# Kernel tuning notes

Measured on AMD Instinct MI355X. Metric: run time of the kernel, lower is better.

The kernel has to match this reference:

```python
import jax, jax.numpy as jnp
import numpy as np

N = 50000          # number of parent nodes / neighborhoods
D_IN = 256         # input_size
K = 8              # points decoded per neighborhood
GLOBAL_DIMS = [256, 128, 64]
FC_DIMS = [256, 256, 256]


def _linear_params(key, d_in, d_out):
    kw, kb = jax.random.split(key)
    W = jax.random.normal(kw, (d_in, d_out), dtype=jnp.float32) * 0.05
    b = jax.random.normal(kb, (d_out,), dtype=jnp.float32) * 0.05
    return W, b


def setup_inputs() -> dict:
    key = jax.random.key(0)
    keys = jax.random.split(key, 8)
    inp = {"input_features": jax.random.normal(keys[0], (N, D_IN), dtype=jnp.float32)}
    # global MLP: 256 -> 256 -> 128 -> 64
    d = D_IN
    for i, nb in enumerate(GLOBAL_DIMS):
        W, b = _linear_params(keys[1 + i], d, nb)
        inp[f"Wg{i}"], inp[f"bg{i}"] = W, b
        d = nb
    # neighborhood decoder head: 64 -> K*3
    inp["Wdec"], inp["bdec"] = _linear_params(keys[4], GLOBAL_DIMS[-1], K * 3)
    # per-point MLP: (256 + 64 + 3) -> 256 -> 256 -> 256
    d = D_IN + GLOBAL_DIMS[-1] + 3
    for i, nb in enumerate(FC_DIMS):
        W, b = _linear_params(keys[5 + i], d, nb)
        inp[f"W{i}"], inp[f"b{i}"] = W, b
        d = nb
    return inp


def reference(input_features, Wg0, bg0, Wg1, bg1, Wg2, bg2, Wdec, bdec,
              W0, b0, W1, b1, W2, b2):
    relu = jax.nn.relu
    # global feature MLP on node features: [N, 256] -> [N, 64]
    feats = input_features
    for W, b in ((Wg0, bg0), (Wg1, bg1), (Wg2, bg2)):
        feats = relu(feats @ W + b)
    # neighborhood decoder: K relative 3D points per node -> [N*K, 3]
    relative_points = (feats @ Wdec + bdec).reshape(-1, 3)
    cluster = jnp.repeat(jnp.arange(N, dtype=jnp.int32), K)  # [N*K]
    # gather (duplicate) parent features per decoded point
    nbr_dup = jnp.take(feats, cluster, axis=0)               # [N*K, 64]
    inp_dup = jnp.take(input_features, cluster, axis=0)      # [N*K, 256]
    decoded = jnp.concatenate([inp_dup, nbr_dup, relative_points], axis=1)  # [N*K, 323]
    for W, b in ((W0, b0), (W1, b1), (W2, b2)):
        decoded = relu(decoded @ W + b)
    return relative_points, decoded, cluster
```

## Files before the change

### kernel.cpp

```cpp
#include <hip/hip_runtime.h>
#include <hip/hip_bf16.h>

typedef __attribute__((ext_vector_type(8))) __bf16 bf16x8;
typedef __attribute__((ext_vector_type(4))) float f32x4;
typedef __attribute__((ext_vector_type(4))) unsigned short u16x4;

#define NN 50000
#define TM1 16
#define PNODES 16

#define FEATS_OFF 212992
#define GW_OFF    3412992

__device__ __forceinline__ unsigned short f2bf(float f) {
    unsigned int u = __builtin_bit_cast(unsigned int, f);
    u = (u + 0x7FFFu + ((u >> 16) & 1u)) >> 16;
    return (unsigned short)u;
}
__device__ __forceinline__ float bf2f(unsigned short h) {
    return __builtin_bit_cast(float, (unsigned int)h << 16);
}

__global__ __launch_bounds__(256) void k_prep(
    const float* __restrict__ W0, const float* __restrict__ W1,
    const float* __restrict__ W2,
    const float* __restrict__ Wg0, const float* __restrict__ Wg1,
    const float* __restrict__ Wg2,
    unsigned short* __restrict__ wbf)
{
    int idx = blockIdx.x * 256 + threadIdx.x;
    if (idx < 81920) {
        int n = idx / 320, k = idx - n * 320;
        wbf[idx] = f2bf(W0[(size_t)k * 256 + n]);
    } else if (idx < 147456) {
        int e = idx - 81920;
        int n = e >> 8, k = e & 255;
        wbf[idx] = f2bf(W1[(size_t)k * 256 + n]);
    } else if (idx < 212992) {
        int e = idx - 147456;
        int n = e >> 8, k = e & 255;
        wbf[idx] = f2bf(W2[(size_t)k * 256 + n]);
    } else if (idx < 319488) {
        int e = idx - 212992;
        float v; int oh, ol;
        if (e < 65536) {
            int n = e >> 8, k = e & 255;
            v = Wg0[(size_t)k * 256 + n];
            oh = GW_OFF + e; ol = GW_OFF + 65536 + e;
        } else if (e < 98304) {
            int e2 = e - 65536;
            int n = e2 >> 8, k = e2 & 255;
            v = Wg1[(size_t)k * 128 + n];
            oh = GW_OFF + 131072 + e2; ol = GW_OFF + 163840 + e2;
        } else {
            int e3 = e - 98304;
            int n = e3 >> 7, k = e3 & 127;
            v = Wg2[(size_t)k * 64 + n];
            oh = GW_OFF + 196608 + e3; ol = GW_OFF + 204800 + e3;
        }
        unsigned short h = f2bf(v);
        wbf[oh] = h;
        wbf[ol] = f2bf(v - bf2f(h));
    }
}

__global__ __launch_bounds__(256, 6) void k_global(
    const float* __restrict__ x,
    const float* __restrict__ bg0, const float* __restrict__ bg1,
    const float* __restrict__ bg2,
    const float* __restrict__ Wdec, const float* __restrict__ bdec,
    const unsigned short* __restrict__ gw,
    unsigned short* __restrict__ feats_bf,
    float* __restrict__ out_rel,
    float* __restrict__ out_cluster)
{
    __shared__ __attribute__((aligned(16))) unsigned char smem[25600];
    unsigned short* bufA = (unsigned short*)(smem);
    unsigned short* bufB = (unsigned short*)(smem + 8448);
    unsigned short* q1h  = (unsigned short*)(smem + 16896);
    unsigned short* q1l  = (unsigned short*)(smem + 21248);
    float*          g2   = (float*)(smem + 16896);

    const int tid  = threadIdx.x;
    const int lane = tid & 63;
    const int w    = tid >> 6;
    const int quad = lane >> 4;
    const int l15  = lane & 15;
    const int blk  = blockIdx.x;

    {
        const float4* xg = (const float4*)(x + (size_t)blk * TM1 * 256);
        #pragma unroll
        for (int it = 0; it < 4; ++it) {
            int e = tid + it * 256;
            int r = e >> 6, c4 = e & 63;
            float4 v = xg[e];
            u16x4 hv, lv;
            hv[0] = f2bf(v.x); lv[0] = f2bf(v.x - bf2f(hv[0]));
            hv[1] = f2bf(v.y); lv[1] = f2bf(v.y - bf2f(hv[1]));
            hv[2] = f2bf(v.z); lv[2] = f2bf(v.z - bf2f(hv[2]));
            hv[3] = f2bf(v.w); lv[3] = f2bf(v.w - bf2f(hv[3]));
            *(u16x4*)&bufA[r * 264 + c4 * 4] = hv;
            *(u16x4*)&bufB[r * 264 + c4 * 4] = lv;
        }
    }
    __syncthreads();

    f32x4 accL0[4];
    {
        const unsigned short* Wh = gw;
        const unsigned short* Wl = gw + 65536;
        f32x4 z = {0.f, 0.f, 0.f, 0.f};
        #pragma unroll
        for (int t = 0; t < 4; ++t) accL0[t] = z;
        #pragma unroll
        for (int ks = 0; ks < 8; ++ks) {
            int k0 = ks * 32 + quad * 8;
            bf16x8 ah = *(const bf16x8*)&bufA[l15 * 264 + k0];
            bf16x8 al = *(const bf16x8*)&bufB[l15 * 264 + k0];
            bf16x8 bh[4], bl[4];
            #pragma unroll
            for (int t = 0; t < 4; ++t) {
                int n = w * 64 + t * 16 + l15;
                bh[t] = *(const bf16x8*)(Wh + (size_t)n * 256 + k0);
                bl[t] = *(const bf16x8*)(Wl + (size_t)n * 256 + k0);
            }
            #pragma unroll
            for (int t = 0; t < 4; ++t) {
                accL0[t] = __builtin_amdgcn_mfma_f32_16x16x32_bf16(ah, bh[t], accL0[t], 0, 0, 0);
                accL0[t] = __builtin_amdgcn_mfma_f32_16x16x32_bf16(al, bh[t], accL0[t], 0, 0, 0);
                accL0[t] = __builtin_amdgcn_mfma_f32_16x16x32_bf16(ah, bl[t], accL0[t], 0, 0, 0);
            }
        }
    }
    __syncthreads();

    {
        #pragma unroll
        for (int t = 0; t < 4; ++t) {
            int col = w * 64 + t * 16 + l15;
            float bb = bg0[col];
            #pragma unroll
            for (int r = 0; r < 4; ++r) {
                int row = quad * 4 + r;
                float v = fmaxf(accL0[t][r] + bb, 0.f);
                unsigned short h = f2bf(v);
                bufA[row * 264 + col] = h;
                bufB[row * 264 + col] = f2bf(v - bf2f(h));
            }
        }
    }
    __syncthreads();

    {
        const unsigned short* Wh = gw + 131072;
        const unsigned short* Wl = gw + 163840;
        f32x4 acc[2];
        f32x4 z = {0.f, 0.f, 0.f, 0.f};
        acc[0] = z; acc[1] = z;
        #pragma unroll
        for (int ks = 0; ks < 8; ++ks) {
            int k0 = ks * 32 + quad * 8;
            bf16x8 ah = *(const bf16x8*)&bufA[l15 * 264 + k0];
            bf16x8 al = *(const bf16x8*)&bufB[l15 * 264 + k0];
            bf16x8 bh[2], bl[2];
            #pragma unroll
            for (int t = 0; t < 2; ++t) {
                int n = w * 32 + t * 16 + l15;
                bh[t] = *(const bf16x8*)(Wh + (size_t)n * 256 + k0);
                bl[t] = *(const bf16x8*)(Wl + (size_t)n * 256 + k0);
            }
            #pragma unroll
            for (int t = 0; t < 2; ++t) {
                acc[t] = __builtin_amdgcn_mfma_f32_16x16x32_bf16(ah, bh[t], acc[t], 0, 0, 0);
                acc[t] = __builtin_amdgcn_mfma_f32_16x16x32_bf16(al, bh[t], acc[t], 0, 0, 0);
                acc[t] = __builtin_amdgcn_mfma_f32_16x16x32_bf16(ah, bl[t], acc[t], 0, 0, 0);
            }
        }
        #pragma unroll
        for (int t = 0; t < 2; ++t) {
            int col = w * 32 + t * 16 + l15;
            float bb = bg1[col];
            #pragma unroll
            for (int r = 0; r < 4; ++r) {
                int row = quad * 4 + r;
                float v = fmaxf(acc[t][r] + bb, 0.f);
                unsigned short h = f2bf(v);
                q1h[row * 136 + col] = h;
                q1l[row * 136 + col] = f2bf(v - bf2f(h));
            }
        }
    }
    __syncthreads();

    f32x4 accL2;
    {
        const unsigned short* Wh = gw + 196608;
        const unsigned short* Wl = gw + 204800;
        f32x4 z = {0.f, 0.f, 0.f, 0.f};
        accL2 = z;
        #pragma unroll
        for (int ks = 0; ks < 4; ++ks) {
            int k0 = ks * 32 + quad * 8;
            bf16x8 ah = *(const bf16x8*)&q1h[l15 * 136 + k0];
            bf16x8 al = *(const bf16x8*)&q1l[l15 * 136 + k0];
            int n = w * 16 + l15;
            bf16x8 bh = *(const bf16x8*)(Wh + (size_t)n * 128 + k0);
            bf16x8 bl = *(const bf16x8*)(Wl + (size_t)n * 128 + k0);
            accL2 = __builtin_amdgcn_mfma_f32_16x16x32_bf16(ah, bh, accL2, 0, 0, 0);
            accL2 = __builtin_amdgcn_mfma_f32_16x16x32_bf16(al, bh, accL2, 0, 0, 0);
            accL2 = __builtin_amdgcn_mfma_f32_16x16x32_bf16(ah, bl, accL2, 0, 0, 0);
        }
    }
    __syncthreads();

    {
        int col = w * 16 + l15;
        float bb = bg2[col];
        #pragma unroll
        for (int r = 0; r < 4; ++r) {
            int row = quad * 4 + r;
            g2[row * 64 + col] = fmaxf(accL2[r] + bb, 0.f);
        }
    }
    __syncthreads();

    {
        const float* src = g2 + tid * 4;
        u16x4 p;
        p[0] = f2bf(src[0]); p[1] = f2bf(src[1]);
        p[2] = f2bf(src[2]); p[3] = f2bf(src[3]);
        *(u16x4*)&feats_bf[(size_t)blk * (TM1 * 64) + tid * 4] = p;
    }

    for (int tt = tid; tt < TM1 * 24; tt += 256) {
        int m = tt / 24;
        int c = tt - m * 24;
        float acc = bdec[c];
        for (int i = 0; i < 64; ++i) acc += g2[m * 64 + i] * Wdec[i * 24 + c];
        out_rel[(size_t)blk * (TM1 * 24) + tt] = acc;
    }

    if (tid < TM1 * 8) {
        out_cluster[(size_t)blk * (TM1 * 8) + tid] = (float)(blk * TM1 + (tid >> 3));
    }
}

__global__ __launch_bounds__(512, 4) void k_points(
    const float* __restrict__ x,
    const unsigned short* __restrict__ feats_bf,
    const float* __restrict__ rel_in,
    const unsigned short* __restrict__ wbf,
    const float* __restrict__ W0f,
    const float* __restrict__ b0,
    const float* __restrict__ b1,
    const float* __restrict__ b2,
    float* __restrict__ out_dec)
{
    __shared__ __attribute__((aligned(16))) unsigned char smem[70144];
    unsigned char*  hB   = smem;
    unsigned short* xcat = (unsigned short*)smem;
    float*          sp   = (float*)(smem + 49152);
    float*          w3   = (float*)(smem + 65536);
    float*          rl   = (float*)(smem + 68608);

    const int tid  = threadIdx.x;
    const int lane = tid & 63;
    const int w    = tid >> 6;
    const int wr   = w >> 2;
    const int wc   = w & 3;
    const int quad = lane >> 4;
    const int l15  = lane & 15;
    const int blk  = blockIdx.x;
    const size_t nb = (size_t)blk * PNODES;

    {
        const float4* xg = (const float4*)(x + nb * 256);
        #pragma unroll
        for (int it = 0; it < 2; ++it) {
            int e = tid + it * 512;
            int r = e >> 6, c4 = e & 63;
            float4 v = xg[e];
            u16x4 hv;
            hv[0] = f2bf(v.x); hv[1] = f2bf(v.y);
            hv[2] = f2bf(v.z); hv[3] = f2bf(v.w);
            *(u16x4*)&xcat[r * 336 + c4 * 4] = hv;
        }
        {
            int e = tid * 2;
            int r = e >> 6, c = e & 63;
            *(unsigned int*)&xcat[r * 336 + 256 + c] =
                *(const unsigned int*)&feats_bf[nb * 64 + e];
        }
        for (int e = tid; e < 768; e += 512)
            w3[e] = W0f[(size_t)(320 + (e >> 8)) * 256 + (e & 255)];
        if (tid < 384) rl[tid] = rel_in[nb * 24 + tid];
    }
    __syncthreads();

    {
        const unsigned short* W0t = wbf;
        f32x4 acc[2];
        f32x4 z = {0.f, 0.f, 0.f, 0.f};
        acc[0] = z; acc[1] = z;
        bf16x8 bcur[2], bnxt[2];
        #pragma unroll
        for (int t = 0; t < 2; ++t)
            bcur[t] = *(const bf16x8*)(W0t + (size_t)(w * 32 + t * 16 + l15) * 320 + quad * 8);
        #pragma unroll
        for (int ks = 0; ks < 10; ++ks) {
            int k0 = ks * 32 + quad * 8;
            bf16x8 a = *(const bf16x8*)&xcat[l15 * 336 + k0];
            if (ks < 9) {
                #pragma unroll
                for (int t = 0; t < 2; ++t)
                    bnxt[t] = *(const bf16x8*)(W0t + (size_t)(w * 32 + t * 16 + l15) * 320 + k0 + 32);
            }
            #pragma unroll
            for (int t = 0; t < 2; ++t)
                acc[t] = __builtin_amdgcn_mfma_f32_16x16x32_bf16(a, bcur[t], acc[t], 0, 0, 0);
            if (ks < 9) {
                #pragma unroll
                for (int t = 0; t < 2; ++t) bcur[t] = bnxt[t];
            }
        }
        #pragma unroll
        for (int t = 0; t < 2; ++t) {
            int col = w * 32 + t * 16 + l15;
            float bb = b0[col];
            #pragma unroll
            for (int r = 0; r < 4; ++r) {
                int row = quad * 4 + r;
                sp[row * 256 + col] = acc[t][r] + bb;
            }
        }
    }
    __syncthreads();

    {
        float4 sv0 = *(const float4*)&sp[(2 * w) * 256 + lane * 4];
        float4 sv1 = *(const float4*)&sp[(2 * w + 1) * 256 + lane * 4];
        float4 wa  = *(const float4*)&w3[lane * 4];
        float4 wb4 = *(const float4*)&w3[256 + lane * 4];
        float4 wc4 = *(const float4*)&w3[512 + lane * 4];
        __syncthreads();
        #pragma unroll
        for (int it = 0; it < 16; ++it) {
            int row  = w * 16 + it;
            int node = 2 * w + (it >> 3);
            int p    = it & 7;
            float4 sv = (it < 8) ? sv0 : sv1;
            float ra = rl[node * 24 + p * 3 + 0];
            float rb = rl[node * 24 + p * 3 + 1];
            float rc = rl[node * 24 + p * 3 + 2];
            float v0 = fmaxf(sv.x + ra * wa.x + rb * wb4.x + rc * wc4.x, 0.f);
            float v1 = fmaxf(sv.y + ra * wa.y + rb * wb4.y + rc * wc4.y, 0.f);
            float v2 = fmaxf(sv.z + ra * wa.z + rb * wb4.z + rc * wc4.z, 0.f);
            float v3 = fmaxf(sv.w + ra * wa.w + rb * wb4.w + rc * wc4.w, 0.f);
            unsigned int lo = (unsigned int)f2bf(v0) | ((unsigned int)f2bf(v1) << 16);
            unsigned int hi = (unsigned int)f2bf(v2) | ((unsigned int)f2bf(v3) << 16);
            uint2 pk; pk.x = lo; pk.y = hi;
            int byteoff = row * 512 +
                ((((lane >> 1) ^ (row & 7)) << 4) | ((lane & 1) << 3));
            *(uint2*)(hB + byteoff) = pk;
        }
    }
    __syncthreads();

    {
        const unsigned short* W1t = wbf + 81920;
        f32x4 acc[4][4];
        f32x4 z = {0.f, 0.f, 0.f, 0.f};
        #pragma unroll
        for (int m = 0; m < 4; ++m)
            #pragma unroll
            for (int t = 0; t < 4; ++t) acc[m][t] = z;
        bf16x8 bcur[4], bnxt[4];
        #pragma unroll
        for (int t = 0; t < 4; ++t)
            bcur[t] = *(const bf16x8*)(W1t + (size_t)(wc * 64 + t * 16 + l15) * 256 + quad * 8);
        #pragma unroll
        for (int ks = 0; ks < 8; ++ks) {
            int k0 = ks * 32 + quad * 8;
            int g  = k0 >> 3;
            bf16x8 a[4];
            #pragma unroll
            for (int m = 0; m < 4; ++m) {
                int row = wr * 64 + m * 16 + l15;
                a[m] = *(const bf16x8*)(hB + row * 512 + ((g ^ (row & 7)) << 4));
            }
            if (ks < 7) {
                #pragma unroll
                for (int t = 0; t < 4; ++t)
                    bnxt[t] = *(const bf16x8*)(W1t + (size_t)(wc * 64 + t * 16 + l15) * 256 + k0 + 32);
            }
            #pragma unroll
            for (int m = 0; m < 4; ++m)
                #pragma unroll
                for (int t = 0; t < 4; ++t)
                    acc[m][t] = __builtin_amdgcn_mfma_f32_16x16x32_bf16(a[m], bcur[t], acc[m][t], 0, 0, 0);
            if (ks < 7) {
                #pragma unroll
                for (int t = 0; t < 4; ++t) bcur[t] = bnxt[t];
            }
        }
        __syncthreads();
        #pragma unroll
        for (int t = 0; t < 4; ++t) {
            int col = wc * 64 + t * 16 + l15;
            float bb = b1[col];
            #pragma unroll
            for (int m = 0; m < 4; ++m) {
                #pragma unroll
                for (int r = 0; r < 4; ++r) {
                    int row = wr * 64 + m * 16 + quad * 4 + r;
                    int byteoff = row * 512 +
                        ((((col >> 3) ^ (row & 7)) << 4) | ((col & 7) << 1));
                    *(unsigned short*)(hB + byteoff) =
                        f2bf(fmaxf(acc[m][t][r] + bb, 0.f));
                }
            }
        }
    }
    __syncthreads();

    {
        const unsigned short* W2t = wbf + 147456;
        f32x4 acc[4][4];
        f32x4 z = {0.f, 0.f, 0.f, 0.f};
        #pragma unroll
        for (int m = 0; m < 4; ++m)
            #pragma unroll
            for (int t = 0; t < 4; ++t) acc[m][t] = z;
        bf16x8 bcur[4], bnxt[4];
        #pragma unroll
        for (int t = 0; t < 4; ++t)
            bcur[t] = *(const bf16x8*)(W2t + (size_t)(wc * 64 + t * 16 + l15) * 256 + quad * 8);
        #pragma unroll
        for (int ks = 0; ks < 8; ++ks) {
            int k0 = ks * 32 + quad * 8;
            int g  = k0 >> 3;
            bf16x8 a[4];
            #pragma unroll
            for (int m = 0; m < 4; ++m) {
                int row = wr * 64 + m * 16 + l15;
                a[m] = *(const bf16x8*)(hB + row * 512 + ((g ^ (row & 7)) << 4));
            }
            if (ks < 7) {
                #pragma unroll
                for (int t = 0; t < 4; ++t)
                    bnxt[t] = *(const bf16x8*)(W2t + (size_t)(wc * 64 + t * 16 + l15) * 256 + k0 + 32);
            }
            #pragma unroll
            for (int m = 0; m < 4; ++m)
                #pragma unroll
                for (int t = 0; t < 4; ++t)
                    acc[m][t] = __builtin_amdgcn_mfma_f32_16x16x32_bf16(a[m], bcur[t], acc[m][t], 0, 0, 0);
            if (ks < 7) {
                #pragma unroll
                for (int t = 0; t < 4; ++t) bcur[t] = bnxt[t];
            }
        }
        #pragma unroll
        for (int t = 0; t < 4; ++t) {
            int col = wc * 64 + t * 16 + l15;
            float bb = b2[col];
            #pragma unroll
            for (int m = 0; m < 4; ++m) {
                #pragma unroll
                for (int r = 0; r < 4; ++r) {
                    int row = wr * 64 + m * 16 + quad * 4 + r;
                    out_dec[((size_t)blk * 128 + row) * 256 + col] =
                        fmaxf(acc[m][t][r] + bb, 0.f);
                }
            }
        }
    }
}

extern "C" void kernel_launch(void* const* d_in, const int* in_sizes, int n_in,
                              void* d_out, int out_size, void* d_ws, size_t ws_size,
                              hipStream_t stream) {
    const float* x    = (const float*)d_in[0];
    const float* Wg0  = (const float*)d_in[1];
    const float* bg0  = (const float*)d_in[2];
    const float* Wg1  = (const float*)d_in[3];
    const float* bg1  = (const float*)d_in[4];
    const float* Wg2  = (const float*)d_in[5];
    const float* bg2  = (const float*)d_in[6];
    const float* Wdec = (const float*)d_in[7];
    const float* bdec = (const float*)d_in[8];
    const float* W0   = (const float*)d_in[9];
    const float* b0   = (const float*)d_in[10];
    const float* W1   = (const float*)d_in[11];
    const float* b1   = (const float*)d_in[12];
    const float* W2   = (const float*)d_in[13];
    const float* b2   = (const float*)d_in[14];

    float* out      = (float*)d_out;
    float* out_rel  = out;
    float* out_dec  = out + 1200000;
    float* out_clu  = out + 103600000;

    unsigned short* wbf      = (unsigned short*)d_ws;
    unsigned short* feats_bf = wbf + FEATS_OFF;
    unsigned short* gw       = wbf + GW_OFF;

    k_prep<<<1248, 256, 0, stream>>>(W0, W1, W2, Wg0, Wg1, Wg2, wbf);
    k_global<<<NN / TM1, 256, 0, stream>>>(x, bg0, bg1, bg2, Wdec, bdec, gw,
                                           feats_bf, out_rel, out_clu);
    k_points<<<NN / PNODES, 512, 0, stream>>>(x, feats_bf, out_rel,
                                              wbf, W0, b0, b1, b2, out_dec);
}
```

Measured before the change: 876.5 us.

## Give each wave its own 16-node tile in global MLP, removing block barriers

The global MLP kernel now assigns a full 16-node tile to each wavefront, and each wave computes every output column with private LDS buffers. Before, the block's four waves split the columns of one shared tile. This removes all __syncthreads between layers and cuts the grid to 782 blocks. The trade-offs are far more accumulator registers per wave (16 tiles for layer 0), launch bounds lowered to allow that, larger shared memory per block, and every wave re-reading the full weight matrices from cache. The decoder dot product is also vectorized with float4 reads of g2.

```diff
diff --git a/kernel.cpp b/kernel.cpp
--- a/kernel.cpp
+++ b/kernel.cpp
@@ -6,7 +6,6 @@
 typedef __attribute__((ext_vector_type(4))) unsigned short u16x4;
 
 #define NN 50000
-#define TM1 16
 #define PNODES 16
 
 #define FEATS_OFF 212992
@@ -64,7 +63,7 @@
     }
 }
 
-__global__ __launch_bounds__(256, 6) void k_global(
+__global__ __launch_bounds__(256, 2) void k_global(
     const float* __restrict__ x,
     const float* __restrict__ bg0, const float* __restrict__ bg1,
     const float* __restrict__ bg2,
@@ -74,25 +73,26 @@
     float* __restrict__ out_rel,
     float* __restrict__ out_cluster)
 {
-    __shared__ __attribute__((aligned(16))) unsigned char smem[25600];
-    unsigned short* bufA = (unsigned short*)(smem);
-    unsigned short* bufB = (unsigned short*)(smem + 8448);
-    unsigned short* q1h  = (unsigned short*)(smem + 16896);
-    unsigned short* q1l  = (unsigned short*)(smem + 21248);
-    float*          g2   = (float*)(smem + 16896);
+    __shared__ __attribute__((aligned(16))) unsigned char smem[67584];
 
     const int tid  = threadIdx.x;
     const int lane = tid & 63;
     const int w    = tid >> 6;
     const int quad = lane >> 4;
     const int l15  = lane & 15;
-    const int blk  = blockIdx.x;
-
-    {
-        const float4* xg = (const float4*)(x + (size_t)blk * TM1 * 256);
-        #pragma unroll
-        for (int it = 0; it < 4; ++it) {
-            int e = tid + it * 256;
+    const int gwid = blockIdx.x * 4 + w;
+    if (gwid >= 3125) return;
+    const size_t node_base = (size_t)gwid * 16;
+
+    unsigned char* wbase = smem + (size_t)w * 16896;
+    unsigned short* A = (unsigned short*)wbase;
+    unsigned short* B = (unsigned short*)(wbase + 8448);
+
+    {
+        const float4* xg = (const float4*)(x + node_base * 256);
+        #pragma unroll
+        for (int it = 0; it < 16; ++it) {
+            int e = lane + it * 64;
             int r = e >> 6, c4 = e & 63;
             float4 v = xg[e];
             u16x4 hv, lv;
@@ -100,149 +100,147 @@
             hv[1] = f2bf(v.y); lv[1] = f2bf(v.y - bf2f(hv[1]));
             hv[2] = f2bf(v.z); lv[2] = f2bf(v.z - bf2f(hv[2]));
             hv[3] = f2bf(v.w); lv[3] = f2bf(v.w - bf2f(hv[3]));
-            *(u16x4*)&bufA[r * 264 + c4 * 4] = hv;
-            *(u16x4*)&bufB[r * 264 + c4 * 4] = lv;
-        }
-    }
-    __syncthreads();
-
-    f32x4 accL0[4];
+            *(u16x4*)&A[r * 264 + c4 * 4] = hv;
+            *(u16x4*)&B[r * 264 + c4 * 4] = lv;
+        }
+    }
+
     {
         const unsigned short* Wh = gw;
         const unsigned short* Wl = gw + 65536;
+        f32x4 acc[16];
         f32x4 z = {0.f, 0.f, 0.f, 0.f};
         #pragma unroll
-        for (int t = 0; t < 4; ++t) accL0[t] = z;
-        #pragma unroll
+        for (int t = 0; t < 16; ++t) acc[t] = z;
+        #pragma unroll 2
         for (int ks = 0; ks < 8; ++ks) {
             int k0 = ks * 32 + quad * 8;
-            bf16x8 ah = *(const bf16x8*)&bufA[l15 * 264 + k0];
-            bf16x8 al = *(const bf16x8*)&bufB[l15 * 264 + k0];
-            bf16x8 bh[4], bl[4];
-            #pragma unroll
-            for (int t = 0; t < 4; ++t) {
-                int n = w * 64 + t * 16 + l15;
-                bh[t] = *(const bf16x8*)(Wh + (size_t)n * 256 + k0);
-                bl[t] = *(const bf16x8*)(Wl + (size_t)n * 256 + k0);
-            }
-            #pragma unroll
-            for (int t = 0; t < 4; ++t) {
-                accL0[t] = __builtin_amdgcn_mfma_f32_16x16x32_bf16(ah, bh[t], accL0[t], 0, 0, 0);
-                accL0[t] = __builtin_amdgcn_mfma_f32_16x16x32_bf16(al, bh[t], accL0[t], 0, 0, 0);
-                accL0[t] = __builtin_amdgcn_mfma_f32_16x16x32_bf16(ah, bl[t], accL0[t], 0, 0, 0);
-            }
-        }
-    }
-    __syncthreads();
-
-    {
-        #pragma unroll
-        for (int t = 0; t < 4; ++t) {
-            int col = w * 64 + t * 16 + l15;
+            bf16x8 ah = *(const bf16x8*)&A[l15 * 264 + k0];
+            bf16x8 al = *(const bf16x8*)&B[l15 * 264 + k0];
+            #pragma unroll
+            for (int t = 0; t < 16; ++t) {
+                int n = t * 16 + l15;
+                bf16x8 bh = *(const bf16x8*)(Wh + (size_t)n * 256 + k0);
+                bf16x8 bl = *(const bf16x8*)(Wl + (size_t)n * 256 + k0);
+                acc[t] = __builtin_amdgcn_mfma_f32_16x16x32_bf16(ah, bh, acc[t], 0, 0, 0);
+                acc[t] = __builtin_amdgcn_mfma_f32_16x16x32_bf16(al, bh, acc[t], 0, 0, 0);
+                acc[t] = __builtin_amdgcn_mfma_f32_16x16x32_bf16(ah, bl, acc[t], 0, 0, 0);
+            }
+        }
+        #pragma unroll
+        for (int t = 0; t < 16; ++t) {
+            int col = t * 16 + l15;
             float bb = bg0[col];
-            #pragma unroll
-            for (int r = 0; r < 4; ++r) {
-                int row = quad * 4 + r;
-                float v = fmaxf(accL0[t][r] + bb, 0.f);
-                unsigned short h = f2bf(v);
-                bufA[row * 264 + col] = h;
-                bufB[row * 264 + col] = f2bf(v - bf2f(h));
-            }
-        }
-    }
-    __syncthreads();
-
-    {
-        const unsigned short* Wh = gw + 131072;
-        const unsigned short* Wl = gw + 163840;
-        f32x4 acc[2];
-        f32x4 z = {0.f, 0.f, 0.f, 0.f};
-        acc[0] = z; acc[1] = z;
-        #pragma unroll
-        for (int ks = 0; ks < 8; ++ks) {
-            int k0 = ks * 32 + quad * 8;
-            bf16x8 ah = *(const bf16x8*)&bufA[l15 * 264 + k0];
-            bf16x8 al = *(const bf16x8*)&bufB[l15 * 264 + k0];
-            bf16x8 bh[2], bl[2];
-            #pragma unroll
-            for (int t = 0; t < 2; ++t) {
-                int n = w * 32 + t * 16 + l15;
-                bh[t] = *(const bf16x8*)(Wh + (size_t)n * 256 + k0);
-                bl[t] = *(const bf16x8*)(Wl + (size_t)n * 256 + k0);
-            }
-            #pragma unroll
-            for (int t = 0; t < 2; ++t) {
-                acc[t] = __builtin_amdgcn_mfma_f32_16x16x32_bf16(ah, bh[t], acc[t], 0, 0, 0);
-                acc[t] = __builtin_amdgcn_mfma_f32_16x16x32_bf16(al, bh[t], acc[t], 0, 0, 0);
-                acc[t] = __builtin_amdgcn_mfma_f32_16x16x32_bf16(ah, bl[t], acc[t], 0, 0, 0);
-            }
-        }
-        #pragma unroll
-        for (int t = 0; t < 2; ++t) {
-            int col = w * 32 + t * 16 + l15;
-            float bb = bg1[col];
             #pragma unroll
             for (int r = 0; r < 4; ++r) {
                 int row = quad * 4 + r;
                 float v = fmaxf(acc[t][r] + bb, 0.f);
                 unsigned short h = f2bf(v);
-                q1h[row * 136 + col] = h;
-                q1l[row * 136 + col] = f2bf(v - bf2f(h));
-            }
-        }
-    }
-    __syncthreads();
-
-    f32x4 accL2;
+                A[row * 264 + col] = h;
+                B[row * 264 + col] = f2bf(v - bf2f(h));
+            }
+        }
+    }
+
+    {
+        const unsigned short* Wh = gw + 131072;
+        const unsigned short* Wl = gw + 163840;
+        f32x4 acc[8];
+        f32x4 z = {0.f, 0.f, 0.f, 0.f};
+        #pragma unroll
+        for (int t = 0; t < 8; ++t) acc[t] = z;
+        #pragma unroll 2
+        for (int ks = 0; ks < 8; ++ks) {
+            int k0 = ks * 32 + quad * 8;
+            bf16x8 ah = *(const bf16x8*)&A[l15 * 264 + k0];
+            bf16x8 al = *(const bf16x8*)&B[l15 * 264 + k0];
+            #pragma unroll
+            for (int t = 0; t < 8; ++t) {
+                int n = t * 16 + l15;
+                bf16x8 bh = *(const bf16x8*)(Wh + (size_t)n * 256 + k0);
+                bf16x8 bl = *(const bf16x8*)(Wl + (size_t)n * 256 + k0);
+                acc[t] = __builtin_amdgcn_mfma_f32_16x16x32_bf16(ah, bh, acc[t], 0, 0, 0);
+                acc[t] = __builtin_amdgcn_mfma_f32_16x16x32_bf16(al, bh, acc[t], 0, 0, 0);
+                acc[t] = __builtin_amdgcn_mfma_f32_16x16x32_bf16(ah, bl, acc[t], 0, 0, 0);
+            }
+        }
+        #pragma unroll
+        for (int t = 0; t < 8; ++t) {
+            int col = t * 16 + l15;
+            float bb = bg1[col];
+            #pragma unroll
+            for (int r = 0; r < 4; ++r) {
+                int row = quad * 4 + r;
+                float v = fmaxf(acc[t][r] + bb, 0.f);
+                unsigned short h = f2bf(v);
+                A[row * 136 + col] = h;
+                B[row * 136 + col] = f2bf(v - bf2f(h));
+            }
+        }
+    }
+
+    float* g2 = (float*)B;
     {
         const unsigned short* Wh = gw + 196608;
         const unsigned short* Wl = gw + 204800;
+        f32x4 acc[4];
         f32x4 z = {0.f, 0.f, 0.f, 0.f};
-        accL2 = z;
+        #pragma unroll
+        for (int t = 0; t < 4; ++t) acc[t] = z;
         #pragma unroll
         for (int ks = 0; ks < 4; ++ks) {
             int k0 = ks * 32 + quad * 8;
-            bf16x8 ah = *(const bf16x8*)&q1h[l15 * 136 + k0];
-            bf16x8 al = *(const bf16x8*)&q1l[l15 * 136 + k0];
-            int n = w * 16 + l15;
-            bf16x8 bh = *(const bf16x8*)(Wh + (size_t)n * 128 + k0);
-            bf16x8 bl = *(const bf16x8*)(Wl + (size_t)n * 128 + k0);
-            accL2 = __builtin_amdgcn_mfma_f32_16x16x32_bf16(ah, bh, accL2, 0, 0, 0);
-            accL2 = __builtin_amdgcn_mfma_f32_16x16x32_bf16(al, bh, accL2, 0, 0, 0);
-            accL2 = __builtin_amdgcn_mfma_f32_16x16x32_bf16(ah, bl, accL2, 0, 0, 0);
-        }
-    }
-    __syncthreads();
-
-    {
-        int col = w * 16 + l15;
-        float bb = bg2[col];
-        #pragma unroll
-        for (int r = 0; r < 4; ++r) {
-            int row = quad * 4 + r;
-            g2[row * 64 + col] = fmaxf(accL2[r] + bb, 0.f);
-        }
-    }
-    __syncthreads();
-
-    {
-        const float* src = g2 + tid * 4;
+            bf16x8 ah = *(const bf16x8*)&A[l15 * 136 + k0];
+            bf16x8 al = *(const bf16x8*)&B[l15 * 136 + k0];
+            #pragma unroll
+            for (int t = 0; t < 4; ++t) {
+                int n = t * 16 + l15;
+                bf16x8 bh = *(const bf16x8*)(Wh + (size_t)n * 128 + k0);
+                bf16x8 bl = *(const bf16x8*)(Wl + (size_t)n * 128 + k0);
+                acc[t] = __builtin_amdgcn_mfma_f32_16x16x32_bf16(ah, bh, acc[t], 0, 0, 0);
+                acc[t] = __builtin_amdgcn_mfma_f32_16x16x32_bf16(al, bh, acc[t], 0, 0, 0);
+                acc[t] = __builtin_amdgcn_mfma_f32_16x16x32_bf16(ah, bl, acc[t], 0, 0, 0);
+            }
+        }
+        #pragma unroll
+        for (int t = 0; t < 4; ++t) {
+            int col = t * 16 + l15;
+            float bb = bg2[col];
+            #pragma unroll
+            for (int r = 0; r < 4; ++r) {
+                int row = quad * 4 + r;
+                g2[row * 64 + col] = fmaxf(acc[t][r] + bb, 0.f);
+            }
+        }
+    }
+
+    #pragma unroll
+    for (int i = 0; i < 4; ++i) {
+        int e4 = lane + i * 64;
+        const float* src = g2 + e4 * 4;
         u16x4 p;
         p[0] = f2bf(src[0]); p[1] = f2bf(src[1]);
         p[2] = f2bf(src[2]); p[3] = f2bf(src[3]);
-        *(u16x4*)&feats_bf[(size_t)blk * (TM1 * 64) + tid * 4] = p;
-    }
-
-    for (int tt = tid; tt < TM1 * 24; tt += 256) {
-        int m = tt / 24;
-        int c = tt - m * 24;
+        *(u16x4*)&feats_bf[node_base * 64 + e4 * 4] = p;
+    }
+
+    #pragma unroll
+    for (int i = 0; i < 6; ++i) {
+        int tt = lane + i * 64;
+        int m = tt / 24, c = tt - m * 24;
         float acc = bdec[c];
-        for (int i = 0; i < 64; ++i) acc += g2[m * 64 + i] * Wdec[i * 24 + c];
-        out_rel[(size_t)blk * (TM1 * 24) + tt] = acc;
-    }
-
-    if (tid < TM1 * 8) {
-        out_cluster[(size_t)blk * (TM1 * 8) + tid] = (float)(blk * TM1 + (tid >> 3));
+        for (int k = 0; k < 64; k += 4) {
+            float4 gv = *(const float4*)&g2[m * 64 + k];
+            acc += gv.x * Wdec[(k + 0) * 24 + c] + gv.y * Wdec[(k + 1) * 24 + c]
+                 + gv.z * Wdec[(k + 2) * 24 + c] + gv.w * Wdec[(k + 3) * 24 + c];
+        }
+        out_rel[node_base * 24 + tt] = acc;
+    }
+
+    #pragma unroll
+    for (int i = 0; i < 2; ++i) {
+        int j = lane + i * 64;
+        out_cluster[node_base * 8 + j] = (float)(node_base + (j >> 3));
     }
 }
 
@@ -507,8 +505,8 @@
     unsigned short* gw       = wbf + GW_OFF;
 
     k_prep<<<1248, 256, 0, stream>>>(W0, W1, W2, Wg0, Wg1, Wg2, wbf);
-    k_global<<<NN / TM1, 256, 0, stream>>>(x, bg0, bg1, bg2, Wdec, bdec, gw,
-                                           feats_bf, out_rel, out_clu);
+    k_global<<<782, 256, 0, stream>>>(x, bg0, bg1, bg2, Wdec, bdec, gw,
+                                      feats_bf, out_rel, out_clu);
     k_points<<<NN / PNODES, 512, 0, stream>>>(x, feats_bf, out_rel,
                                               wbf, W0, b0, b1, b2, out_dec);
 }
```

Result: slower. 903.2 us (+3.0%).

## Prefetch next-layer weights across barriers and double-buffer global MLP smem

Applied to the files above, without the earlier changes.

In the global MLP kernel, each layer's weights and biases are now loaded into registers before the preceding barrier and software-pipelined across k-steps. Separate shared buffers for the input and hidden activations remove one barrier per layer. The point-MLP kernel likewise issues the first weight fragments of the next layer before each barrier and reorders global weight loads ahead of the LDS loads. Together these aim to hide global weight-load latency behind barriers and MFMA work, at the cost of more registers and LDS, with occupancy lowered from 6 to 4 blocks per CU.

```diff
diff --git a/kernel.cpp b/kernel.cpp
--- a/kernel.cpp
+++ b/kernel.cpp
@@ -64,7 +64,7 @@
     }
 }
 
-__global__ __launch_bounds__(256, 6) void k_global(
+__global__ __launch_bounds__(256, 4) void k_global(
     const float* __restrict__ x,
     const float* __restrict__ bg0, const float* __restrict__ bg1,
     const float* __restrict__ bg2,
@@ -74,12 +74,14 @@
     float* __restrict__ out_rel,
     float* __restrict__ out_cluster)
 {
-    __shared__ __attribute__((aligned(16))) unsigned char smem[25600];
-    unsigned short* bufA = (unsigned short*)(smem);
-    unsigned short* bufB = (unsigned short*)(smem + 8448);
-    unsigned short* q1h  = (unsigned short*)(smem + 16896);
-    unsigned short* q1l  = (unsigned short*)(smem + 21248);
-    float*          g2   = (float*)(smem + 16896);
+    __shared__ __attribute__((aligned(16))) unsigned char smem[37888];
+    unsigned short* xh  = (unsigned short*)(smem);
+    unsigned short* xl  = (unsigned short*)(smem + 8448);
+    unsigned short* q1h = (unsigned short*)(smem);
+    unsigned short* q1l = (unsigned short*)(smem + 4352);
+    unsigned short* hh  = (unsigned short*)(smem + 16896);
+    unsigned short* hl  = (unsigned short*)(smem + 25344);
+    float*          g2  = (float*)(smem + 33792);
 
     const int tid  = threadIdx.x;
     const int lane = tid & 63;
@@ -87,6 +89,18 @@
     const int quad = lane >> 4;
     const int l15  = lane & 15;
     const int blk  = blockIdx.x;
+
+    const unsigned short* W0h = gw;
+    const unsigned short* W0l = gw + 65536;
+    bf16x8 bcur0[4], bnxt0[4];
+    float bias0[4];
+    #pragma unroll
+    for (int t = 0; t < 4; ++t) {
+        int n = w * 64 + t * 16 + l15;
+        bcur0[t] = *(const bf16x8*)(W0h + (size_t)n * 256 + quad * 8);
+        bnxt0[t] = *(const bf16x8*)(W0l + (size_t)n * 256 + quad * 8);
+        bias0[t] = bg0[n];
+    }
 
     {
         const float4* xg = (const float4*)(x + (size_t)blk * TM1 * 256);
@@ -100,76 +114,87 @@
             hv[1] = f2bf(v.y); lv[1] = f2bf(v.y - bf2f(hv[1]));
             hv[2] = f2bf(v.z); lv[2] = f2bf(v.z - bf2f(hv[2]));
             hv[3] = f2bf(v.w); lv[3] = f2bf(v.w - bf2f(hv[3]));
-            *(u16x4*)&bufA[r * 264 + c4 * 4] = hv;
-            *(u16x4*)&bufB[r * 264 + c4 * 4] = lv;
-        }
-    }
-    __syncthreads();
-
-    f32x4 accL0[4];
-    {
-        const unsigned short* Wh = gw;
-        const unsigned short* Wl = gw + 65536;
+            *(u16x4*)&xh[r * 264 + c4 * 4] = hv;
+            *(u16x4*)&xl[r * 264 + c4 * 4] = lv;
+        }
+    }
+    __syncthreads();
+
+    {
+        f32x4 acc[4];
         f32x4 z = {0.f, 0.f, 0.f, 0.f};
         #pragma unroll
-        for (int t = 0; t < 4; ++t) accL0[t] = z;
+        for (int t = 0; t < 4; ++t) acc[t] = z;
         #pragma unroll
         for (int ks = 0; ks < 8; ++ks) {
             int k0 = ks * 32 + quad * 8;
-            bf16x8 ah = *(const bf16x8*)&bufA[l15 * 264 + k0];
-            bf16x8 al = *(const bf16x8*)&bufB[l15 * 264 + k0];
             bf16x8 bh[4], bl[4];
             #pragma unroll
+            for (int t = 0; t < 4; ++t) { bh[t] = bcur0[t]; bl[t] = bnxt0[t]; }
+            if (ks < 7) {
+                #pragma unroll
+                for (int t = 0; t < 4; ++t) {
+                    int n = w * 64 + t * 16 + l15;
+                    bcur0[t] = *(const bf16x8*)(W0h + (size_t)n * 256 + k0 + 32);
+                    bnxt0[t] = *(const bf16x8*)(W0l + (size_t)n * 256 + k0 + 32);
+                }
+            }
+            bf16x8 ah = *(const bf16x8*)&xh[l15 * 264 + k0];
+            bf16x8 al = *(const bf16x8*)&xl[l15 * 264 + k0];
+            #pragma unroll
             for (int t = 0; t < 4; ++t) {
-                int n = w * 64 + t * 16 + l15;
-                bh[t] = *(const bf16x8*)(Wh + (size_t)n * 256 + k0);
-                bl[t] = *(const bf16x8*)(Wl + (size_t)n * 256 + k0);
-            }
-            #pragma unroll
-            for (int t = 0; t < 4; ++t) {
-                accL0[t] = __builtin_amdgcn_mfma_f32_16x16x32_bf16(ah, bh[t], accL0[t], 0, 0, 0);
-                accL0[t] = __builtin_amdgcn_mfma_f32_16x16x32_bf16(al, bh[t], accL0[t], 0, 0, 0);
-                accL0[t] = __builtin_amdgcn_mfma_f32_16x16x32_bf16(ah, bl[t], accL0[t], 0, 0, 0);
-            }
-        }
-    }
-    __syncthreads();
-
-    {
+                acc[t] = __builtin_amdgcn_mfma_f32_16x16x32_bf16(ah, bh[t], acc[t], 0, 0, 0);
+                acc[t] = __builtin_amdgcn_mfma_f32_16x16x32_bf16(al, bh[t], acc[t], 0, 0, 0);
+                acc[t] = __builtin_amdgcn_mfma_f32_16x16x32_bf16(ah, bl[t], acc[t], 0, 0, 0);
+            }
+        }
         #pragma unroll
         for (int t = 0; t < 4; ++t) {
             int col = w * 64 + t * 16 + l15;
-            float bb = bg0[col];
             #pragma unroll
             for (int r = 0; r < 4; ++r) {
                 int row = quad * 4 + r;
-                float v = fmaxf(accL0[t][r] + bb, 0.f);
+                float v = fmaxf(acc[t][r] + bias0[t], 0.f);
                 unsigned short h = f2bf(v);
-                bufA[row * 264 + col] = h;
-                bufB[row * 264 + col] = f2bf(v - bf2f(h));
-            }
-        }
-    }
-    __syncthreads();
-
-    {
-        const unsigned short* Wh = gw + 131072;
-        const unsigned short* Wl = gw + 163840;
+                hh[row * 264 + col] = h;
+                hl[row * 264 + col] = f2bf(v - bf2f(h));
+            }
+        }
+    }
+
+    const unsigned short* W1h = gw + 131072;
+    const unsigned short* W1l = gw + 163840;
+    bf16x8 bcur1[2], bnxt1[2];
+    float bias1[2];
+    #pragma unroll
+    for (int t = 0; t < 2; ++t) {
+        int n = w * 32 + t * 16 + l15;
+        bcur1[t] = *(const bf16x8*)(W1h + (size_t)n * 256 + quad * 8);
+        bnxt1[t] = *(const bf16x8*)(W1l + (size_t)n * 256 + quad * 8);
+        bias1[t] = bg1[n];
+    }
+    __syncthreads();
+
+    {
         f32x4 acc[2];
         f32x4 z = {0.f, 0.f, 0.f, 0.f};
         acc[0] = z; acc[1] = z;
         #pragma unroll
         for (int ks = 0; ks < 8; ++ks) {
             int k0 = ks * 32 + quad * 8;
-            bf16x8 ah = *(const bf16x8*)&bufA[l15 * 264 + k0];
-            bf16x8 al = *(const bf16x8*)&bufB[l15 * 264 + k0];
             bf16x8 bh[2], bl[2];
             #pragma unroll
-            for (int t = 0; t < 2; ++t) {
-                int n = w * 32 + t * 16 + l15;
-                bh[t] = *(const bf16x8*)(Wh + (size_t)n * 256 + k0);
-                bl[t] = *(const bf16x8*)(Wl + (size_t)n * 256 + k0);
-            }
+            for (int t = 0; t < 2; ++t) { bh[t] = bcur1[t]; bl[t] = bnxt1[t]; }
+            if (ks < 7) {
+                #pragma unroll
+                for (int t = 0; t < 2; ++t) {
+                    int n = w * 32 + t * 16 + l15;
+                    bcur1[t] = *(const bf16x8*)(W1h + (size_t)n * 256 + k0 + 32);
+                    bnxt1[t] = *(const bf16x8*)(W1l + (size_t)n * 256 + k0 + 32);
+                }
+            }
+            bf16x8 ah = *(const bf16x8*)&hh[l15 * 264 + k0];
+            bf16x8 al = *(const bf16x8*)&hl[l15 * 264 + k0];
             #pragma unroll
             for (int t = 0; t < 2; ++t) {
                 acc[t] = __builtin_amdgcn_mfma_f32_16x16x32_bf16(ah, bh[t], acc[t], 0, 0, 0);
@@ -180,47 +205,49 @@
         #pragma unroll
         for (int t = 0; t < 2; ++t) {
             int col = w * 32 + t * 16 + l15;
-            float bb = bg1[col];
             #pragma unroll
             for (int r = 0; r < 4; ++r) {
                 int row = quad * 4 + r;
-                float v = fmaxf(acc[t][r] + bb, 0.f);
+                float v = fmaxf(acc[t][r] + bias1[t], 0.f);
                 unsigned short h = f2bf(v);
                 q1h[row * 136 + col] = h;
                 q1l[row * 136 + col] = f2bf(v - bf2f(h));
             }
         }
     }
-    __syncthreads();
-
-    f32x4 accL2;
-    {
-        const unsigned short* Wh = gw + 196608;
-        const unsigned short* Wl = gw + 204800;
-        f32x4 z = {0.f, 0.f, 0.f, 0.f};
-        accL2 = z;
+
+    const unsigned short* W2h = gw + 196608;
+    const unsigned short* W2l = gw + 204800;
+    bf16x8 c2h[4], c2l[4];
+    float bias2;
+    {
+        int n = w * 16 + l15;
+        #pragma unroll
+        for (int ks = 0; ks < 4; ++ks) {
+            int k0 = ks * 32 + quad * 8;
+            c2h[ks] = *(const bf16x8*)(W2h + (size_t)n * 128 + k0);
+            c2l[ks] = *(const bf16x8*)(W2l + (size_t)n * 128 + k0);
+        }
+        bias2 = bg2[n];
+    }
+    __syncthreads();
+
+    {
+        f32x4 acc = {0.f, 0.f, 0.f, 0.f};
         #pragma unroll
         for (int ks = 0; ks < 4; ++ks) {
             int k0 = ks * 32 + quad * 8;
             bf16x8 ah = *(const bf16x8*)&q1h[l15 * 136 + k0];
             bf16x8 al = *(const bf16x8*)&q1l[l15 * 136 + k0];
-            int n = w * 16 + l15;
-            bf16x8 bh = *(const bf16x8*)(Wh + (size_t)n * 128 + k0);
-            bf16x8 bl = *(const bf16x8*)(Wl + (size_t)n * 128 + k0);
-            accL2 = __builtin_amdgcn_mfma_f32_16x16x32_bf16(ah, bh, accL2, 0, 0, 0);
-            accL2 = __builtin_amdgcn_mfma_f32_16x16x32_bf16(al, bh, accL2, 0, 0, 0);
-            accL2 = __builtin_amdgcn_mfma_f32_16x16x32_bf16(ah, bl, accL2, 0, 0, 0);
-        }
-    }
-    __syncthreads();
-
-    {
+            acc = __builtin_amdgcn_mfma_f32_16x16x32_bf16(ah, c2h[ks], acc, 0, 0, 0);
+            acc = __builtin_amdgcn_mfma_f32_16x16x32_bf16(al, c2h[ks], acc, 0, 0, 0);
+            acc = __builtin_amdgcn_mfma_f32_16x16x32_bf16(ah, c2l[ks], acc, 0, 0, 0);
+        }
         int col = w * 16 + l15;
-        float bb = bg2[col];
         #pragma unroll
         for (int r = 0; r < 4; ++r) {
             int row = quad * 4 + r;
-            g2[row * 64 + col] = fmaxf(accL2[r] + bb, 0.f);
+            g2[row * 64 + col] = fmaxf(acc[r] + bias2, 0.f);
         }
     }
     __syncthreads();
@@ -237,7 +264,11 @@
         int m = tt / 24;
         int c = tt - m * 24;
         float acc = bdec[c];
-        for (int i = 0; i < 64; ++i) acc += g2[m * 64 + i] * Wdec[i * 24 + c];
+        for (int i = 0; i < 64; i += 4) {
+            float4 gv = *(const float4*)&g2[m * 64 + i];
+            acc += gv.x * Wdec[(i + 0) * 24 + c] + gv.y * Wdec[(i + 1) * 24 + c]
+                 + gv.z * Wdec[(i + 2) * 24 + c] + gv.w * Wdec[(i + 3) * 24 + c];
+        }
         out_rel[(size_t)blk * (TM1 * 24) + tt] = acc;
     }
 
@@ -310,12 +341,12 @@
         #pragma unroll
         for (int ks = 0; ks < 10; ++ks) {
             int k0 = ks * 32 + quad * 8;
-            bf16x8 a = *(const bf16x8*)&xcat[l15 * 336 + k0];
             if (ks < 9) {
                 #pragma unroll
                 for (int t = 0; t < 2; ++t)
                     bnxt[t] = *(const bf16x8*)(W0t + (size_t)(w * 32 + t * 16 + l15) * 320 + k0 + 32);
             }
+            bf16x8 a = *(const bf16x8*)&xcat[l15 * 336 + k0];
             #pragma unroll
             for (int t = 0; t < 2; ++t)
                 acc[t] = __builtin_amdgcn_mfma_f32_16x16x32_bf16(a, bcur[t], acc[t], 0, 0, 0);
@@ -335,6 +366,12 @@
             }
         }
     }
+
+    const unsigned short* W1t = wbf + 81920;
+    bf16x8 f1cur[4];
+    #pragma unroll
+    for (int t = 0; t < 4; ++t)
+        f1cur[t] = *(const bf16x8*)(W1t + (size_t)(wc * 64 + t * 16 + l15) * 256 + quad * 8);
     __syncthreads();
 
     {
@@ -368,42 +405,42 @@
     __syncthreads();
 
     {
-        const unsigned short* W1t = wbf + 81920;
         f32x4 acc[4][4];
         f32x4 z = {0.f, 0.f, 0.f, 0.f};
         #pragma unroll
         for (int m = 0; m < 4; ++m)
             #pragma unroll
             for (int t = 0; t < 4; ++t) acc[m][t] = z;
-        bf16x8 bcur[4], bnxt[4];
-        #pragma unroll
-        for (int t = 0; t < 4; ++t)
-            bcur[t] = *(const bf16x8*)(W1t + (size_t)(wc * 64 + t * 16 + l15) * 256 + quad * 8);
+        bf16x8 bnxt[4];
         #pragma unroll
         for (int ks = 0; ks < 8; ++ks) {
             int k0 = ks * 32 + quad * 8;
             int g  = k0 >> 3;
+            if (ks < 7) {
+                #pragma unroll
+                for (int t = 0; t < 4; ++t)
+                    bnxt[t] = *(const bf16x8*)(W1t + (size_t)(wc * 64 + t * 16 + l15) * 256 + k0 + 32);
+            }
             bf16x8 a[4];
             #pragma unroll
             for (int m = 0; m < 4; ++m) {
                 int row = wr * 64 + m * 16 + l15;
                 a[m] = *(const bf16x8*)(hB + row * 512 + ((g ^ (row & 7)) << 4));
             }
+            #pragma unroll
+            for (int m = 0; m < 4; ++m)
+                #pragma unroll
+                for (int t = 0; t < 4; ++t)
+                    acc[m][t] = __builtin_amdgcn_mfma_f32_16x16x32_bf16(a[m], f1cur[t], acc[m][t], 0, 0, 0);
             if (ks < 7) {
                 #pragma unroll
-                for (int t = 0; t < 4; ++t)
-                    bnxt[t] = *(const bf16x8*)(W1t + (size_t)(wc * 64 + t * 16 + l15) * 256 + k0 + 32);
-            }
-            #pragma unroll
-            for (int m = 0; m < 4; ++m)
-                #pragma unroll
-                for (int t = 0; t < 4; ++t)
-                    acc[m][t] = __builtin_amdgcn_mfma_f32_16x16x32_bf16(a[m], bcur[t], acc[m][t], 0, 0, 0);
-            if (ks < 7) {
-                #pragma unroll
-                for (int t = 0; t < 4; ++t) bcur[t] = bnxt[t];
-            }
-        }
+                for (int t = 0; t < 4; ++t) f1cur[t] = bnxt[t];
+            }
+        }
+        const unsigned short* W2t = wbf + 147456;
+        #pragma unroll
+        for (int t = 0; t < 4; ++t)
+            f1cur[t] = *(const bf16x8*)(W2t + (size_t)(wc * 64 + t * 16 + l15) * 256 + quad * 8);
         __syncthreads();
         #pragma unroll
         for (int t = 0; t < 4; ++t) {
@@ -432,33 +469,30 @@
         for (int m = 0; m < 4; ++m)
             #pragma unroll
             for (int t = 0; t < 4; ++t) acc[m][t] = z;
-        bf16x8 bcur[4], bnxt[4];
-        #pragma unroll
-        for (int t = 0; t < 4; ++t)
-            bcur[t] = *(const bf16x8*)(W2t + (size_t)(wc * 64 + t * 16 + l15) * 256 + quad * 8);
+        bf16x8 bnxt[4];
         #pragma unroll
         for (int ks = 0; ks < 8; ++ks) {
             int k0 = ks * 32 + quad * 8;
             int g  = k0 >> 3;
+            if (ks < 7) {
+                #pragma unroll
+                for (int t = 0; t < 4; ++t)
+                    bnxt[t] = *(const bf16x8*)(W2t + (size_t)(wc * 64 + t * 16 + l15) * 256 + k0 + 32);
+            }
             bf16x8 a[4];
             #pragma unroll
             for (int m = 0; m < 4; ++m) {
                 int row = wr * 64 + m * 16 + l15;
                 a[m] = *(const bf16x8*)(hB + row * 512 + ((g ^ (row & 7)) << 4));
             }
+            #pragma unroll
+            for (int m = 0; m < 4; ++m)
+                #pragma unroll
+                for (int t = 0; t < 4; ++t)
+                    acc[m][t] = __builtin_amdgcn_mfma_f32_16x16x32_bf16(a[m], f1cur[t], acc[m][t], 0, 0, 0);
             if (ks < 7) {
                 #pragma unroll
-                for (int t = 0; t < 4; ++t)
-                    bnxt[t] = *(const bf16x8*)(W2t + (size_t)(wc * 64 + t * 16 + l15) * 256 + k0 + 32);
-            }
-            #pragma unroll
-            for (int m = 0; m < 4; ++m)
-                #pragma unroll
-                for (int t = 0; t < 4; ++t)
-                    acc[m][t] = __builtin_amdgcn_mfma_f32_16x16x32_bf16(a[m], bcur[t], acc[m][t], 0, 0, 0);
-            if (ks < 7) {
-                #pragma unroll
-                for (int t = 0; t < 4; ++t) bcur[t] = bnxt[t];
+                for (int t = 0; t < 4; ++t) f1cur[t] = bnxt[t];
             }
         }
         #pragma unroll
```

Result: slower. 909.9 us (+3.8%).
